# Kernel tuning notes

Hardware: AMD Instinct MI355X
Metric: run time of the kernel (lower is better)

The kernel has to match this reference:

```python
import jax, jax.numpy as jnp
import numpy as np

NEG_SLOPE = 0.01  # torch leaky_relu default
STEPS = 19

def _lrelu(x):
    return jnp.where(x >= 0, x, NEG_SLOPE * x)

def setup_inputs() -> dict:
    key = jax.random.key(0)
    ks = jax.random.split(key, 13)
    def lin(kw, kb, fan_in, fan_out):
        bound = 1.0 / np.sqrt(fan_in)
        W = jax.random.uniform(kw, (fan_in, fan_out), minval=-bound, maxval=bound, dtype=jnp.float32)
        b = jax.random.uniform(kb, (fan_out,), minval=-bound, maxval=bound, dtype=jnp.float32)
        return W, b
    Wh1, bh1 = lin(ks[0], ks[1], 2, 50)
    Wh2, bh2 = lin(ks[2], ks[3], 50, 20)
    Wh3, bh3 = lin(ks[4], ks[5], 20, 2)
    Wz1, bz1 = lin(ks[6], ks[7], 2, 50)
    Wz2, bz2 = lin(ks[8], ks[9], 50, 20)
    Wz3, bz3 = lin(ks[10], ks[11], 20, 2)
    w = jax.random.normal(ks[12], (1048576, 2), dtype=jnp.float32)
    return {"w": w,
            "Wh1": Wh1, "bh1": bh1, "Wh2": Wh2, "bh2": bh2, "Wh3": Wh3, "bh3": bh3,
            "Wz1": Wz1, "bz1": bz1, "Wz2": Wz2, "bz2": bz2, "Wz3": Wz3, "bz3": bz3}

def reference(w, Wh1, bh1, Wh2, bh2, Wh3, bh3, Wz1, bz1, Wz2, bz2, Wz3, bz3):
    def step(h, _):
        h = _lrelu(h @ Wh1 + bh1)          # [B,50]
        h = _lrelu(h @ Wh2 + bh2)          # [B,20]
        h = _lrelu(h @ Wh3 + bh3)          # [B,2]
        z = jax.nn.sigmoid(h @ Wz1 + bz1)  # [B,50]
        z = jax.nn.sigmoid(z @ Wz2 + bz2)  # [B,20]
        z = jax.nn.sigmoid(z @ Wz3 + bz3)  # [B,2]
        return h, z
    _, zs = jax.lax.scan(step, w, None, length=STEPS)  # zs: [19,B,2]
    return jnp.transpose(zs, (1, 0, 2))                # [B,19,2]
```

## Files before the change

### kernel.cpp

```cpp
#include <hip/hip_runtime.h>
#include <math.h>

#define STEPS 19
#define THREADS 256
#define L2E 1.44269504088896340736f

typedef _Float16 half8  __attribute__((ext_vector_type(8)));
typedef float    floatx4 __attribute__((ext_vector_type(4)));
typedef __fp16   half2_t __attribute__((ext_vector_type(2)));

#define ROW_BYTES 144
#define WAVE_LDS  (64 * ROW_BYTES)
#define CSTRIDE   22

#define WS_BH   0
#define WS_BZ   4096
#define WS_WZ1  8192
#define WS_BZ1  8592
#define WS_WZ3  8792
#define WS_BZ3  8952

#define LDS_FENCE() asm volatile("" ::: "memory")

__device__ __forceinline__ float lrelu(float x) { return fmaxf(x, 0.01f * x); }
__device__ __forceinline__ float sigm2(float y) {
    return __builtin_amdgcn_rcpf(1.0f + __builtin_amdgcn_exp2f(y));
}
__device__ __forceinline__ unsigned int pkrtz_u(float a, float b) {
    return __builtin_bit_cast(unsigned int, __builtin_amdgcn_cvt_pkrtz(a, b));
}
__device__ __forceinline__ unsigned int packh2(float a, float b) {
    half2_t h; h.x = (__fp16)a; h.y = (__fp16)b;
    return __builtin_bit_cast(unsigned int, h);
}

__global__ __launch_bounds__(256) void pack_kernel(
    const float* __restrict__ Wh2, const float* __restrict__ bh2,
    const float* __restrict__ Wz1, const float* __restrict__ bz1,
    const float* __restrict__ Wz2, const float* __restrict__ bz2,
    const float* __restrict__ Wz3, const float* __restrict__ bz3,
    char* __restrict__ ws)
{
    const int t = threadIdx.x;
    for (int e = t; e < 512; e += 256) {
        const int layer = e >> 8, r = e & 255;
        const int u = r >> 7, kk = (r >> 6) & 1, lane = r & 63;
        const int n = u * 16 + (lane & 15);
        const float* W2 = layer ? Wz2 : Wh2;
        const float* b2 = layer ? bz2 : bh2;
        const float scale = layer ? -L2E : 1.0f;
        unsigned int dw[4];
        #pragma unroll
        for (int d = 0; d < 4; ++d) {
            float v[2];
            #pragma unroll
            for (int h = 0; h < 2; ++h) {
                const int k = kk * 32 + ((lane >> 4) & 3) * 8 + 2 * d + h;
                float x = 0.0f;
                if (n < 20) {
                    if (k < 50)       x = W2[k * 20 + n] * scale;
                    else if (k == 50) x = b2[n] * scale;
                }
                v[h] = x;
            }
            dw[d] = packh2(v[0], v[1]);
        }
        *(uint4*)(ws + (layer ? WS_BZ : WS_BH) + (size_t)((u * 2 + kk) * 64 + lane) * 16)
            = make_uint4(dw[0], dw[1], dw[2], dw[3]);
    }
    if (t < 100) ((float*)(ws + WS_WZ1))[t] = -L2E * Wz1[t];
    if (t < 50)  ((float*)(ws + WS_BZ1))[t] = -L2E * bz1[t];
    if (t < 40)  ((float*)(ws + WS_WZ3))[t] = -L2E * Wz3[t];
    if (t < 2)   ((float*)(ws + WS_BZ3))[t] = -L2E * bz3[t];
}

__global__ __launch_bounds__(THREADS)
__attribute__((amdgpu_waves_per_eu(2)))
void recurrent_kernel(
    const float* __restrict__ w,
    const float* __restrict__ Wh1, const float* __restrict__ bh1,
    const float* __restrict__ Wh3, const float* __restrict__ bh3,
    const char* __restrict__ ws,
    float* __restrict__ out, int nrows)
{
    __shared__ __align__(16) char lds[4 * WAVE_LDS];
    const int t    = threadIdx.x;
    const int lane = t & 63;
    const int wid  = t >> 6;
    const int lq   = (lane >> 4) & 3;
    const int ll   = lane & 15;
    char* base  = lds + wid * WAVE_LDS;
    char* myrow = base + lane * ROW_BYTES;

    uint4 Bh[2][2], Bz[2][2];
    #pragma unroll
    for (int u = 0; u < 2; ++u)
        #pragma unroll
        for (int kk = 0; kk < 2; ++kk) {
            Bh[u][kk] = *(const uint4*)(ws + WS_BH + (size_t)((u * 2 + kk) * 64 + lane) * 16);
            Bz[u][kk] = *(const uint4*)(ws + WS_BZ + (size_t)((u * 2 + kk) * 64 + lane) * 16);
        }
    const float* Wz1s = (const float*)(ws + WS_WZ1);
    const float* bz1s = (const float*)(ws + WS_BZ1);
    const float* Wz3s = (const float*)(ws + WS_WZ3);
    const float* bz3s = (const float*)(ws + WS_BZ3);

    const int row = blockIdx.x * THREADS + t;
    const bool ok = row < nrows;
    const int rr  = ok ? row : 0;
    const float2 w2 = *(const float2*)(w + 2 * (size_t)rr);
    float h0 = w2.x, h1 = w2.y;
    float* orow = out + (size_t)row * (STEPS * 2);

    #pragma unroll 1
    for (int s = 0; s < STEPS; ++s) {
        #pragma unroll
        for (int b = 0; b < 6; ++b) {
            float av[8];
            #pragma unroll
            for (int j = 0; j < 8; ++j) {
                const int k = b * 8 + j;
                av[j] = lrelu(fmaf(h1, Wh1[50 + k], fmaf(h0, Wh1[k], bh1[k])));
            }
            *(uint4*)(myrow + b * 16) = make_uint4(
                pkrtz_u(av[0], av[1]), pkrtz_u(av[2], av[3]),
                pkrtz_u(av[4], av[5]), pkrtz_u(av[6], av[7]));
        }
        {
            const float a48 = lrelu(fmaf(h1, Wh1[98], fmaf(h0, Wh1[48], bh1[48])));
            const float a49 = lrelu(fmaf(h1, Wh1[99], fmaf(h0, Wh1[49], bh1[49])));
            *(uint4*)(myrow + 96)  = make_uint4(pkrtz_u(a48, a49), pkrtz_u(1.0f, 0.0f), 0u, 0u);
            *(uint4*)(myrow + 112) = make_uint4(0u, 0u, 0u, 0u);
        }
        LDS_FENCE();
        floatx4 C[4][2];
        #pragma unroll
        for (int mt = 0; mt < 4; ++mt) { C[mt][0] = (floatx4)0.0f; C[mt][1] = (floatx4)0.0f; }
        #pragma unroll
        for (int mt = 0; mt < 4; ++mt) {
            const char* ab = base + (mt * 16 + ll) * ROW_BYTES + lq * 16;
            const half8 A0 = __builtin_bit_cast(half8, *(const uint4*)(ab));
            const half8 A1 = __builtin_bit_cast(half8, *(const uint4*)(ab + 64));
            C[mt][0] = __builtin_amdgcn_mfma_f32_16x16x32_f16(A0, __builtin_bit_cast(half8, Bh[0][0]), C[mt][0], 0, 0, 0);
            C[mt][1] = __builtin_amdgcn_mfma_f32_16x16x32_f16(A0, __builtin_bit_cast(half8, Bh[1][0]), C[mt][1], 0, 0, 0);
            C[mt][0] = __builtin_amdgcn_mfma_f32_16x16x32_f16(A1, __builtin_bit_cast(half8, Bh[0][1]), C[mt][0], 0, 0, 0);
            C[mt][1] = __builtin_amdgcn_mfma_f32_16x16x32_f16(A1, __builtin_bit_cast(half8, Bh[1][1]), C[mt][1], 0, 0, 0);
        }
        LDS_FENCE();
        #pragma unroll
        for (int mt = 0; mt < 4; ++mt)
            #pragma unroll
            for (int u = 0; u < 2; ++u)
                #pragma unroll
                for (int i = 0; i < 4; ++i)
                    *(float*)(base + (size_t)(((mt * 16 + lq * 4 + i) * CSTRIDE) + u * 16 + ll) * 4) = C[mt][u][i];
        LDS_FENCE();
        float a2[20];
        #pragma unroll
        for (int p = 0; p < 10; ++p) {
            const float2 v = *(const float2*)(base + (size_t)(lane * CSTRIDE + 2 * p) * 4);
            a2[2 * p] = v.x; a2[2 * p + 1] = v.y;
        }
        LDS_FENCE();
        float nh0 = bh3[0], nh1 = bh3[1];
        #pragma unroll
        for (int i = 0; i < 20; ++i) {
            const float a = lrelu(a2[i]);
            nh0 = fmaf(a, Wh3[2 * i], nh0);
            nh1 = fmaf(a, Wh3[2 * i + 1], nh1);
        }
        h0 = lrelu(nh0); h1 = lrelu(nh1);

        #pragma unroll
        for (int b = 0; b < 6; ++b) {
            float zv[8];
            #pragma unroll
            for (int j = 0; j < 8; ++j) {
                const int k = b * 8 + j;
                zv[j] = sigm2(fmaf(h1, Wz1s[50 + k], fmaf(h0, Wz1s[k], bz1s[k])));
            }
            *(uint4*)(myrow + b * 16) = make_uint4(
                pkrtz_u(zv[0], zv[1]), pkrtz_u(zv[2], zv[3]),
                pkrtz_u(zv[4], zv[5]), pkrtz_u(zv[6], zv[7]));
        }
        {
            const float z48 = sigm2(fmaf(h1, Wz1s[98], fmaf(h0, Wz1s[48], bz1s[48])));
            const float z49 = sigm2(fmaf(h1, Wz1s[99], fmaf(h0, Wz1s[49], bz1s[49])));
            *(uint4*)(myrow + 96)  = make_uint4(pkrtz_u(z48, z49), pkrtz_u(1.0f, 0.0f), 0u, 0u);
            *(uint4*)(myrow + 112) = make_uint4(0u, 0u, 0u, 0u);
        }
        LDS_FENCE();
        #pragma unroll
        for (int mt = 0; mt < 4; ++mt) { C[mt][0] = (floatx4)0.0f; C[mt][1] = (floatx4)0.0f; }
        #pragma unroll
        for (int mt = 0; mt < 4; ++mt) {
            const char* ab = base + (mt * 16 + ll) * ROW_BYTES + lq * 16;
            const half8 A0 = __builtin_bit_cast(half8, *(const uint4*)(ab));
            const half8 A1 = __builtin_bit_cast(half8, *(const uint4*)(ab + 64));
            C[mt][0] = __builtin_amdgcn_mfma_f32_16x16x32_f16(A0, __builtin_bit_cast(half8, Bz[0][0]), C[mt][0], 0, 0, 0);
            C[mt][1] = __builtin_amdgcn_mfma_f32_16x16x32_f16(A0, __builtin_bit_cast(half8, Bz[1][0]), C[mt][1], 0, 0, 0);
            C[mt][0] = __builtin_amdgcn_mfma_f32_16x16x32_f16(A1, __builtin_bit_cast(half8, Bz[0][1]), C[mt][0], 0, 0, 0);
            C[mt][1] = __builtin_amdgcn_mfma_f32_16x16x32_f16(A1, __builtin_bit_cast(half8, Bz[1][1]), C[mt][1], 0, 0, 0);
        }
        LDS_FENCE();
        #pragma unroll
        for (int mt = 0; mt < 4; ++mt)
            #pragma unroll
            for (int u = 0; u < 2; ++u)
                #pragma unroll
                for (int i = 0; i < 4; ++i)
                    *(float*)(base + (size_t)(((mt * 16 + lq * 4 + i) * CSTRIDE) + u * 16 + ll) * 4) = C[mt][u][i];
        LDS_FENCE();
        #pragma unroll
        for (int p = 0; p < 10; ++p) {
            const float2 v = *(const float2*)(base + (size_t)(lane * CSTRIDE + 2 * p) * 4);
            a2[2 * p] = v.x; a2[2 * p + 1] = v.y;
        }
        LDS_FENCE();
        float zo0 = bz3s[0], zo1 = bz3s[1];
        #pragma unroll
        for (int i = 0; i < 20; ++i) {
            const float zz = sigm2(a2[i]);
            zo0 = fmaf(zz, Wz3s[2 * i], zo0);
            zo1 = fmaf(zz, Wz3s[2 * i + 1], zo1);
        }
        if (ok) {
            float2 o; o.x = sigm2(zo0); o.y = sigm2(zo1);
            *(float2*)(orow + 2 * s) = o;
        }
    }
}

extern "C" void kernel_launch(void* const* d_in, const int* in_sizes, int n_in,
                              void* d_out, int out_size, void* d_ws, size_t ws_size,
                              hipStream_t stream) {
    const float* w   = (const float*)d_in[0];
    const float* Wh1 = (const float*)d_in[1];
    const float* bh1 = (const float*)d_in[2];
    const float* Wh2 = (const float*)d_in[3];
    const float* bh2 = (const float*)d_in[4];
    const float* Wh3 = (const float*)d_in[5];
    const float* bh3 = (const float*)d_in[6];
    const float* Wz1 = (const float*)d_in[7];
    const float* bz1 = (const float*)d_in[8];
    const float* Wz2 = (const float*)d_in[9];
    const float* bz2 = (const float*)d_in[10];
    const float* Wz3 = (const float*)d_in[11];
    const float* bz3 = (const float*)d_in[12];
    float* out = (float*)d_out;

    pack_kernel<<<1, 256, 0, stream>>>(Wh2, bh2, Wz1, bz1, Wz2, bz2, Wz3, bz3,
                                       (char*)d_ws);

    const int nrows = in_sizes[0] / 2;
    const int blocks = (nrows + THREADS - 1) / THREADS;
    recurrent_kernel<<<blocks, THREADS, 0, stream>>>(
        w, Wh1, bh1, Wh3, bh3, (const char*)d_ws, out, nrows);
}
```

Before: 768.2 us.

## Compute h-layer1 in packed fp16 and remap LDS layout to MFMA fragment order

Computes the first h-layer with packed half2 FMAs and max-based leaky ReLU, using fp16 weights prepacked by the pack kernel. This halves the VALU work for that layer at some cost in precision. The A-operand and C-transpose LDS layouts are rearranged so each lane writes and reads contiguous 16-byte chunks in MFMA fragment order, and the C readback uses float4 loads. The intent is to cut LDS bank conflicts and instruction count. MFMA accumulators now start from a zero constant instead of being explicitly cleared.

```diff
diff --git a/kernel.cpp b/kernel.cpp
--- a/kernel.cpp
+++ b/kernel.cpp
@@ -5,20 +5,21 @@
 #define THREADS 256
 #define L2E 1.44269504088896340736f
 
-typedef _Float16 half8  __attribute__((ext_vector_type(8)));
+typedef _Float16 half8   __attribute__((ext_vector_type(8)));
 typedef float    floatx4 __attribute__((ext_vector_type(4)));
 typedef __fp16   half2_t __attribute__((ext_vector_type(2)));
 
-#define ROW_BYTES 144
-#define WAVE_LDS  (64 * ROW_BYTES)
-#define CSTRIDE   22
-
-#define WS_BH   0
-#define WS_BZ   4096
-#define WS_WZ1  8192
-#define WS_BZ1  8592
-#define WS_WZ3  8792
-#define WS_BZ3  8952
+#define WAVE_LDS 8192
+
+#define WS_BH    0
+#define WS_BZ    4096
+#define WS_H1W0  8192
+#define WS_H1W1  8292
+#define WS_H1B   8392
+#define WS_WZ1   8492
+#define WS_BZ1   8892
+#define WS_WZ3   9092
+#define WS_BZ3   9252
 
 #define LDS_FENCE() asm volatile("" ::: "memory")
 
@@ -33,8 +34,15 @@
     half2_t h; h.x = (__fp16)a; h.y = (__fp16)b;
     return __builtin_bit_cast(unsigned int, h);
 }
+__device__ __forceinline__ unsigned int h2bits(half2_t h) {
+    return __builtin_bit_cast(unsigned int, h);
+}
+__device__ __forceinline__ half2_t bits2h(unsigned int u) {
+    return __builtin_bit_cast(half2_t, u);
+}
 
 __global__ __launch_bounds__(256) void pack_kernel(
+    const float* __restrict__ Wh1, const float* __restrict__ bh1,
     const float* __restrict__ Wh2, const float* __restrict__ bh2,
     const float* __restrict__ Wz1, const float* __restrict__ bz1,
     const float* __restrict__ Wz2, const float* __restrict__ bz2,
@@ -68,6 +76,11 @@
         *(uint4*)(ws + (layer ? WS_BZ : WS_BH) + (size_t)((u * 2 + kk) * 64 + lane) * 16)
             = make_uint4(dw[0], dw[1], dw[2], dw[3]);
     }
+    if (t < 25) {
+        ((unsigned int*)(ws + WS_H1W0))[t] = packh2(Wh1[2 * t],      Wh1[2 * t + 1]);
+        ((unsigned int*)(ws + WS_H1W1))[t] = packh2(Wh1[50 + 2 * t], Wh1[51 + 2 * t]);
+        ((unsigned int*)(ws + WS_H1B))[t]  = packh2(bh1[2 * t],      bh1[2 * t + 1]);
+    }
     if (t < 100) ((float*)(ws + WS_WZ1))[t] = -L2E * Wz1[t];
     if (t < 50)  ((float*)(ws + WS_BZ1))[t] = -L2E * bz1[t];
     if (t < 40)  ((float*)(ws + WS_WZ3))[t] = -L2E * Wz3[t];
@@ -78,7 +91,6 @@
 __attribute__((amdgpu_waves_per_eu(2)))
 void recurrent_kernel(
     const float* __restrict__ w,
-    const float* __restrict__ Wh1, const float* __restrict__ bh1,
     const float* __restrict__ Wh3, const float* __restrict__ bh3,
     const char* __restrict__ ws,
     float* __restrict__ out, int nrows)
@@ -89,8 +101,14 @@
     const int wid  = t >> 6;
     const int lq   = (lane >> 4) & 3;
     const int ll   = lane & 15;
-    char* base  = lds + wid * WAVE_LDS;
-    char* myrow = base + lane * ROW_BYTES;
+    char* ldsw = lds + wid * WAVE_LDS;
+
+    char* awb = ldsw + (lane >> 4) * 1024 + (lane & 15) * 16;
+    const char* arb = ldsw + lane * 16;
+    const int cmod = (ll < 4) ? (16 + ll) : (ll - 4);
+    char* cw0 = ldsw + lq * 320 + ll * 4;
+    char* cw1 = ldsw + lq * 320 + cmod * 4;
+    const char* crb = ldsw + lane * 80;
 
     uint4 Bh[2][2], Bz[2][2];
     #pragma unroll
@@ -100,66 +118,78 @@
             Bh[u][kk] = *(const uint4*)(ws + WS_BH + (size_t)((u * 2 + kk) * 64 + lane) * 16);
             Bz[u][kk] = *(const uint4*)(ws + WS_BZ + (size_t)((u * 2 + kk) * 64 + lane) * 16);
         }
+    const unsigned int* W0p = (const unsigned int*)(ws + WS_H1W0);
+    const unsigned int* W1p = (const unsigned int*)(ws + WS_H1W1);
+    const unsigned int* B1p = (const unsigned int*)(ws + WS_H1B);
     const float* Wz1s = (const float*)(ws + WS_WZ1);
     const float* bz1s = (const float*)(ws + WS_BZ1);
     const float* Wz3s = (const float*)(ws + WS_WZ3);
     const float* bz3s = (const float*)(ws + WS_BZ3);
 
+    const half2_t c001h = {(__fp16)0.01f, (__fp16)0.01f};
+    const floatx4 ZC = {0.0f, 0.0f, 0.0f, 0.0f};
+
     const int row = blockIdx.x * THREADS + t;
     const bool ok = row < nrows;
-    const int rr  = ok ? row : 0;
-    const float2 w2 = *(const float2*)(w + 2 * (size_t)rr);
+    const float2 w2 = *(const float2*)(w + 2 * (size_t)(ok ? row : 0));
     float h0 = w2.x, h1 = w2.y;
     float* orow = out + (size_t)row * (STEPS * 2);
 
     #pragma unroll 1
     for (int s = 0; s < STEPS; ++s) {
-        #pragma unroll
-        for (int b = 0; b < 6; ++b) {
-            float av[8];
-            #pragma unroll
-            for (int j = 0; j < 8; ++j) {
-                const int k = b * 8 + j;
-                av[j] = lrelu(fmaf(h1, Wh1[50 + k], fmaf(h0, Wh1[k], bh1[k])));
-            }
-            *(uint4*)(myrow + b * 16) = make_uint4(
-                pkrtz_u(av[0], av[1]), pkrtz_u(av[2], av[3]),
-                pkrtz_u(av[4], av[5]), pkrtz_u(av[6], av[7]));
-        }
         {
-            const float a48 = lrelu(fmaf(h1, Wh1[98], fmaf(h0, Wh1[48], bh1[48])));
-            const float a49 = lrelu(fmaf(h1, Wh1[99], fmaf(h0, Wh1[49], bh1[49])));
-            *(uint4*)(myrow + 96)  = make_uint4(pkrtz_u(a48, a49), pkrtz_u(1.0f, 0.0f), 0u, 0u);
-            *(uint4*)(myrow + 112) = make_uint4(0u, 0u, 0u, 0u);
+            const __fp16 h0h = (__fp16)h0, h1h = (__fp16)h1;
+            const half2_t h00 = {h0h, h0h};
+            const half2_t h11 = {h1h, h1h};
+            #pragma unroll
+            for (int c = 0; c < 6; ++c) {
+                unsigned int dw[4];
+                #pragma unroll
+                for (int p = 0; p < 4; ++p) {
+                    const int q = c * 4 + p;
+                    half2_t v = h11 * bits2h(W1p[q]) + (h00 * bits2h(W0p[q]) + bits2h(B1p[q]));
+                    v = __builtin_elementwise_max(v, v * c001h);
+                    dw[p] = h2bits(v);
+                }
+                *(uint4*)(awb + (c >> 2) * 4096 + (c & 3) * 256)
+                    = make_uint4(dw[0], dw[1], dw[2], dw[3]);
+            }
+            {
+                half2_t v = h11 * bits2h(W1p[24]) + (h00 * bits2h(W0p[24]) + bits2h(B1p[24]));
+                v = __builtin_elementwise_max(v, v * c001h);
+                *(uint4*)(awb + 4096 + 2 * 256) = make_uint4(h2bits(v), 0x00003C00u, 0u, 0u);
+            }
+            *(uint4*)(awb + 4096 + 3 * 256) = make_uint4(0u, 0u, 0u, 0u);
         }
         LDS_FENCE();
         floatx4 C[4][2];
         #pragma unroll
-        for (int mt = 0; mt < 4; ++mt) { C[mt][0] = (floatx4)0.0f; C[mt][1] = (floatx4)0.0f; }
-        #pragma unroll
         for (int mt = 0; mt < 4; ++mt) {
-            const char* ab = base + (mt * 16 + ll) * ROW_BYTES + lq * 16;
-            const half8 A0 = __builtin_bit_cast(half8, *(const uint4*)(ab));
-            const half8 A1 = __builtin_bit_cast(half8, *(const uint4*)(ab + 64));
-            C[mt][0] = __builtin_amdgcn_mfma_f32_16x16x32_f16(A0, __builtin_bit_cast(half8, Bh[0][0]), C[mt][0], 0, 0, 0);
-            C[mt][1] = __builtin_amdgcn_mfma_f32_16x16x32_f16(A0, __builtin_bit_cast(half8, Bh[1][0]), C[mt][1], 0, 0, 0);
+            const half8 A0 = __builtin_bit_cast(half8, *(const uint4*)(arb + mt * 1024));
+            const half8 A1 = __builtin_bit_cast(half8, *(const uint4*)(arb + 4096 + mt * 1024));
+            C[mt][0] = __builtin_amdgcn_mfma_f32_16x16x32_f16(A0, __builtin_bit_cast(half8, Bh[0][0]), ZC,       0, 0, 0);
             C[mt][0] = __builtin_amdgcn_mfma_f32_16x16x32_f16(A1, __builtin_bit_cast(half8, Bh[0][1]), C[mt][0], 0, 0, 0);
+            C[mt][1] = __builtin_amdgcn_mfma_f32_16x16x32_f16(A0, __builtin_bit_cast(half8, Bh[1][0]), ZC,       0, 0, 0);
             C[mt][1] = __builtin_amdgcn_mfma_f32_16x16x32_f16(A1, __builtin_bit_cast(half8, Bh[1][1]), C[mt][1], 0, 0, 0);
         }
         LDS_FENCE();
         #pragma unroll
         for (int mt = 0; mt < 4; ++mt)
             #pragma unroll
-            for (int u = 0; u < 2; ++u)
-                #pragma unroll
-                for (int i = 0; i < 4; ++i)
-                    *(float*)(base + (size_t)(((mt * 16 + lq * 4 + i) * CSTRIDE) + u * 16 + ll) * 4) = C[mt][u][i];
+            for (int i = 0; i < 4; ++i)
+                *(float*)(cw1 + mt * 1280 + i * 80) = C[mt][1][i];
+        LDS_FENCE();
+        #pragma unroll
+        for (int mt = 0; mt < 4; ++mt)
+            #pragma unroll
+            for (int i = 0; i < 4; ++i)
+                *(float*)(cw0 + mt * 1280 + i * 80) = C[mt][0][i];
         LDS_FENCE();
         float a2[20];
         #pragma unroll
-        for (int p = 0; p < 10; ++p) {
-            const float2 v = *(const float2*)(base + (size_t)(lane * CSTRIDE + 2 * p) * 4);
-            a2[2 * p] = v.x; a2[2 * p + 1] = v.y;
+        for (int p = 0; p < 5; ++p) {
+            const float4 v = *(const float4*)(crb + p * 16);
+            a2[4 * p] = v.x; a2[4 * p + 1] = v.y; a2[4 * p + 2] = v.z; a2[4 * p + 3] = v.w;
         }
         LDS_FENCE();
         float nh0 = bh3[0], nh1 = bh3[1];
@@ -172,49 +202,52 @@
         h0 = lrelu(nh0); h1 = lrelu(nh1);
 
         #pragma unroll
-        for (int b = 0; b < 6; ++b) {
-            float zv[8];
-            #pragma unroll
-            for (int j = 0; j < 8; ++j) {
-                const int k = b * 8 + j;
-                zv[j] = sigm2(fmaf(h1, Wz1s[50 + k], fmaf(h0, Wz1s[k], bz1s[k])));
-            }
-            *(uint4*)(myrow + b * 16) = make_uint4(
-                pkrtz_u(zv[0], zv[1]), pkrtz_u(zv[2], zv[3]),
-                pkrtz_u(zv[4], zv[5]), pkrtz_u(zv[6], zv[7]));
+        for (int c = 0; c < 6; ++c) {
+            unsigned int dw[4];
+            #pragma unroll
+            for (int p = 0; p < 4; ++p) {
+                const int k = c * 8 + 2 * p;
+                const float y0 = fmaf(h1, Wz1s[50 + k],     fmaf(h0, Wz1s[k],     bz1s[k]));
+                const float y1 = fmaf(h1, Wz1s[50 + k + 1], fmaf(h0, Wz1s[k + 1], bz1s[k + 1]));
+                dw[p] = pkrtz_u(sigm2(y0), sigm2(y1));
+            }
+            *(uint4*)(awb + (c >> 2) * 4096 + (c & 3) * 256)
+                = make_uint4(dw[0], dw[1], dw[2], dw[3]);
         }
         {
-            const float z48 = sigm2(fmaf(h1, Wz1s[98], fmaf(h0, Wz1s[48], bz1s[48])));
-            const float z49 = sigm2(fmaf(h1, Wz1s[99], fmaf(h0, Wz1s[49], bz1s[49])));
-            *(uint4*)(myrow + 96)  = make_uint4(pkrtz_u(z48, z49), pkrtz_u(1.0f, 0.0f), 0u, 0u);
-            *(uint4*)(myrow + 112) = make_uint4(0u, 0u, 0u, 0u);
-        }
-        LDS_FENCE();
-        #pragma unroll
-        for (int mt = 0; mt < 4; ++mt) { C[mt][0] = (floatx4)0.0f; C[mt][1] = (floatx4)0.0f; }
+            const float y48 = fmaf(h1, Wz1s[98], fmaf(h0, Wz1s[48], bz1s[48]));
+            const float y49 = fmaf(h1, Wz1s[99], fmaf(h0, Wz1s[49], bz1s[49]));
+            *(uint4*)(awb + 4096 + 2 * 256)
+                = make_uint4(pkrtz_u(sigm2(y48), sigm2(y49)), 0x00003C00u, 0u, 0u);
+        }
+        *(uint4*)(awb + 4096 + 3 * 256) = make_uint4(0u, 0u, 0u, 0u);
+        LDS_FENCE();
         #pragma unroll
         for (int mt = 0; mt < 4; ++mt) {
-            const char* ab = base + (mt * 16 + ll) * ROW_BYTES + lq * 16;
-            const half8 A0 = __builtin_bit_cast(half8, *(const uint4*)(ab));
-            const half8 A1 = __builtin_bit_cast(half8, *(const uint4*)(ab + 64));
-            C[mt][0] = __builtin_amdgcn_mfma_f32_16x16x32_f16(A0, __builtin_bit_cast(half8, Bz[0][0]), C[mt][0], 0, 0, 0);
-            C[mt][1] = __builtin_amdgcn_mfma_f32_16x16x32_f16(A0, __builtin_bit_cast(half8, Bz[1][0]), C[mt][1], 0, 0, 0);
+            const half8 A0 = __builtin_bit_cast(half8, *(const uint4*)(arb + mt * 1024));
+            const half8 A1 = __builtin_bit_cast(half8, *(const uint4*)(arb + 4096 + mt * 1024));
+            C[mt][0] = __builtin_amdgcn_mfma_f32_16x16x32_f16(A0, __builtin_bit_cast(half8, Bz[0][0]), ZC,       0, 0, 0);
             C[mt][0] = __builtin_amdgcn_mfma_f32_16x16x32_f16(A1, __builtin_bit_cast(half8, Bz[0][1]), C[mt][0], 0, 0, 0);
+            C[mt][1] = __builtin_amdgcn_mfma_f32_16x16x32_f16(A0, __builtin_bit_cast(half8, Bz[1][0]), ZC,       0, 0, 0);
             C[mt][1] = __builtin_amdgcn_mfma_f32_16x16x32_f16(A1, __builtin_bit_cast(half8, Bz[1][1]), C[mt][1], 0, 0, 0);
         }
         LDS_FENCE();
         #pragma unroll
         for (int mt = 0; mt < 4; ++mt)
             #pragma unroll
-            for (int u = 0; u < 2; ++u)
-                #pragma unroll
-                for (int i = 0; i < 4; ++i)
-                    *(float*)(base + (size_t)(((mt * 16 + lq * 4 + i) * CSTRIDE) + u * 16 + ll) * 4) = C[mt][u][i];
-        LDS_FENCE();
-        #pragma unroll
-        for (int p = 0; p < 10; ++p) {
-            const float2 v = *(const float2*)(base + (size_t)(lane * CSTRIDE + 2 * p) * 4);
-            a2[2 * p] = v.x; a2[2 * p + 1] = v.y;
+            for (int i = 0; i < 4; ++i)
+                *(float*)(cw1 + mt * 1280 + i * 80) = C[mt][1][i];
+        LDS_FENCE();
+        #pragma unroll
+        for (int mt = 0; mt < 4; ++mt)
+            #pragma unroll
+            for (int i = 0; i < 4; ++i)
+                *(float*)(cw0 + mt * 1280 + i * 80) = C[mt][0][i];
+        LDS_FENCE();
+        #pragma unroll
+        for (int p = 0; p < 5; ++p) {
+            const float4 v = *(const float4*)(crb + p * 16);
+            a2[4 * p] = v.x; a2[4 * p + 1] = v.y; a2[4 * p + 2] = v.z; a2[4 * p + 3] = v.w;
         }
         LDS_FENCE();
         float zo0 = bz3s[0], zo1 = bz3s[1];
@@ -249,11 +282,11 @@
     const float* bz3 = (const float*)d_in[12];
     float* out = (float*)d_out;
 
-    pack_kernel<<<1, 256, 0, stream>>>(Wh2, bh2, Wz1, bz1, Wz2, bz2, Wz3, bz3,
-                                       (char*)d_ws);
+    pack_kernel<<<1, 256, 0, stream>>>(Wh1, bh1, Wh2, bh2, Wz1, bz1, Wz2, bz2,
+                                       Wz3, bz3, (char*)d_ws);
 
     const int nrows = in_sizes[0] / 2;
     const int blocks = (nrows + THREADS - 1) / THREADS;
     recurrent_kernel<<<blocks, THREADS, 0, stream>>>(
-        w, Wh1, bh1, Wh3, bh3, (const char*)d_ws, out, nrows);
-}
+        w, Wh3, bh3, (const char*)d_ws, out, nrows);
+}
```

Measured after the change: 671.0 us. -12.7%, faster.
